# Performance work log

Measured on AMD Instinct MI355X. Metric: run time of the kernel, lower is better.

## Reference

```python
import jax, jax.numpy as jnp
import numpy as np

B, S, H = 2, 1024, 1024
N_IN, N_PROC = 512, 32


def _l2norm(x, eps=1e-12):
    n = jnp.linalg.norm(x, axis=-1, keepdims=True)
    return x / jnp.maximum(n, eps)


def setup_inputs() -> dict:
    key = jax.random.key(0)
    k1, k2, k3, k4 = jax.random.split(key, 4)
    intermediate = jax.random.normal(k1, (B, S, H), dtype=jnp.float32)
    input_activations = jax.random.normal(k2, (B, S, N_IN), dtype=jnp.float32)
    # params (torch defaults: pattern_templates ~ randn; Linear weight ~ U scaled)
    pattern_templates = jax.random.normal(k3, (N_PROC, N_IN), dtype=jnp.float32)
    bound = 1.0 / np.sqrt(H)
    W_transform = jax.random.uniform(k4, (N_PROC * H, H), dtype=jnp.float32,
                                     minval=-bound, maxval=bound)
    return {"intermediate": intermediate, "input_activations": input_activations,
            "pattern_templates": pattern_templates, "W_transform": W_transform}


def reference(intermediate, input_activations, pattern_templates, W_transform):
    # pattern matching -> soft routing weights  [B,S,N_proc]
    act_norm = _l2norm(input_activations)
    tmpl_norm = _l2norm(pattern_templates)
    process_activations = jax.nn.sigmoid(
        jnp.einsum('bsi,ni->bsn', act_norm, tmpl_norm))
    # dispatch: weighted sum over sequence (batched GEMM instead of bcast-mul-sum)
    contexts = jnp.einsum('bsh,bsn->bnh', intermediate, process_activations)
    norm = process_activations.sum(axis=1)[..., None] + 1e-8  # [B,N_proc,1]
    contexts = contexts / norm
    # per-process-neuron HxH transform (torch Linear weight is [out,in])
    Wn = W_transform.reshape(N_PROC, H, H)  # [n, k(out), h(in)]
    transformed = jnp.einsum('bnh,nkh->bnk', contexts, Wn)
    # combine back to tokens  [B,S,H]
    combined = jnp.einsum('bnh,bsn->bsh', transformed, process_activations)
    return combined, process_activations
```

## Files before the change

### kernel.cpp

```cpp
#include <hip/hip_runtime.h>
#include <math.h>

#define B 2
#define S 1024
#define H 1024
#define NIN 512
#define NP 32
#define SC 16
#define SCHUNK (S / SC)

__global__ void k_tmpl_norm(const float* __restrict__ tmpl, float* __restrict__ tn) {
    int n = blockIdx.x;
    int lane = threadIdx.x;
    const float* row = tmpl + (size_t)n * NIN;
    float v[8];
    float ss = 0.f;
#pragma unroll
    for (int k = 0; k < 8; ++k) { v[k] = row[lane + 64 * k]; ss += v[k] * v[k]; }
#pragma unroll
    for (int off = 32; off; off >>= 1) ss += __shfl_down(ss, off);
    ss = __shfl(ss, 0);
    float inv = 1.f / fmaxf(sqrtf(ss), 1e-12f);
#pragma unroll
    for (int k = 0; k < 8; ++k) tn[(size_t)n * NIN + lane + 64 * k] = v[k] * inv;
}

__global__ void k_pattern(const float* __restrict__ act, const float* __restrict__ tn,
                          float* __restrict__ P) {
    __shared__ float act_lds[8][NIN];
    int tid = threadIdx.x;
    int t0 = blockIdx.x * 8;
    {
        const float* src = act + (size_t)t0 * NIN;
        float* dst = &act_lds[0][0];
        for (int k = tid; k < 8 * NIN; k += 256) dst[k] = src[k];
    }
    __syncthreads();
    int tok = tid >> 5;
    int n   = tid & 31;
    float ss = 0.f;
#pragma unroll
    for (int k = 0; k < 16; ++k) { float x = act_lds[tok][n + 32 * k]; ss += x * x; }
#pragma unroll
    for (int m = 16; m; m >>= 1) ss += __shfl_xor(ss, m);
    float inv = 1.f / fmaxf(sqrtf(ss), 1e-12f);
    const float4* t4 = (const float4*)(tn + (size_t)n * NIN);
    const float4* a4 = (const float4*)(&act_lds[tok][0]);
    float d = 0.f;
#pragma unroll 8
    for (int i = 0; i < NIN / 4; ++i) {
        float4 tv = t4[i];
        float4 av = a4[i];
        d += tv.x * av.x + tv.y * av.y + tv.z * av.z + tv.w * av.w;
    }
    d *= inv;
    float p = 1.f / (1.f + expf(-d));
    P[(size_t)(t0 + tok) * NP + n] = p;
}

__global__ void k_norm(const float* __restrict__ P, float* __restrict__ nrm) {
    int bn = blockIdx.x;
    int b = bn >> 5, n = bn & 31;
    int tid = threadIdx.x;
    float s = 0.f;
#pragma unroll
    for (int k = 0; k < 4; ++k) {
        int si = tid + 256 * k;
        s += P[((size_t)b * S + si) * NP + n];
    }
    __shared__ float red[256];
    red[tid] = s;
    __syncthreads();
    for (int off = 128; off >= 1; off >>= 1) {
        if (tid < off) red[tid] += red[tid + off];
        __syncthreads();
    }
    if (tid == 0) nrm[bn] = red[0] + 1e-8f;
}

__global__ void k_ctx_partial(const float* __restrict__ I, const float* __restrict__ P,
                              float* __restrict__ part) {
    int bid = blockIdx.x;
    int ht = bid & 7;
    int sc = (bid >> 3) & (SC - 1);
    int b  = bid >> 7;
    int tid = threadIdx.x;
    __shared__ float Pl[SCHUNK][NP];
    int s0 = sc * SCHUNK;
    {
        const float* src = P + ((size_t)b * S + s0) * NP;
        float* dst = &Pl[0][0];
        for (int k = tid; k < SCHUNK * NP; k += 256) dst[k] = src[k];
    }
    __syncthreads();
    int hl = tid & 127;
    int g  = tid >> 7;
    int h  = ht * 128 + hl;
    float acc[16];
#pragma unroll
    for (int j = 0; j < 16; ++j) acc[j] = 0.f;
    const float* Ip = I + ((size_t)b * S + s0) * H + h;
    for (int s = 0; s < SCHUNK; ++s) {
        float x = Ip[(size_t)s * H];
#pragma unroll
        for (int j = 0; j < 16; ++j) acc[j] += x * Pl[s][g * 16 + j];
    }
    size_t base = (((size_t)b * SC + sc) * NP + g * 16) * H + h;
#pragma unroll
    for (int j = 0; j < 16; ++j) part[base + (size_t)j * H] = acc[j];
}

__global__ void k_ctx_reduce(const float* __restrict__ part, const float* __restrict__ nrm,
                             float* __restrict__ ctx) {
    int idx = blockIdx.x * 256 + threadIdx.x;
    int n = (idx >> 10) & 31;
    int b = idx >> 15;
    float s = 0.f;
#pragma unroll
    for (int sc = 0; sc < SC; ++sc)
        s += part[((size_t)(b * SC + sc) * NP + n) * H + (idx & 1023)];
    ctx[idx] = s / nrm[b * NP + n];
}

__global__ void k_transform(const float* __restrict__ W, const float* __restrict__ ctx,
                            float* __restrict__ T) {
    int bid = blockIdx.x;
    int n  = bid >> 8;
    int kg = bid & 255;
    __shared__ float cl[2 * H];
    int tid = threadIdx.x;
    for (int k = tid; k < 2 * H; k += 256) {
        int b = k >> 10, h = k & 1023;
        cl[k] = ctx[((size_t)b * NP + n) * H + h];
    }
    __syncthreads();
    int w = tid >> 6;
    int lane = tid & 63;
    int kk = kg * 4 + w;
    const float4* Wr = (const float4*)(W + ((size_t)n * H + kk) * H);
    const float4* c0 = (const float4*)(cl);
    const float4* c1 = (const float4*)(cl + H);
    float a0 = 0.f, a1 = 0.f;
#pragma unroll
    for (int it = 0; it < 4; ++it) {
        int idx = it * 64 + lane;
        float4 wv = Wr[idx];
        float4 v0 = c0[idx];
        float4 v1 = c1[idx];
        a0 += wv.x * v0.x + wv.y * v0.y + wv.z * v0.z + wv.w * v0.w;
        a1 += wv.x * v1.x + wv.y * v1.y + wv.z * v1.z + wv.w * v1.w;
    }
#pragma unroll
    for (int off = 32; off; off >>= 1) {
        a0 += __shfl_down(a0, off);
        a1 += __shfl_down(a1, off);
    }
    if (lane == 0) {
        T[(size_t)n * H + kk] = a0;
        T[((size_t)NP + n) * H + kk] = a1;
    }
}

__global__ void k_combine(const float* __restrict__ T, const float* __restrict__ P,
                          float* __restrict__ out) {
    int bid = blockIdx.x;
    int ht = bid & 3;
    int sc = (bid >> 2) & 63;
    int b  = bid >> 8;
    int tid = threadIdx.x;
    __shared__ float Tl[NP][256];
    __shared__ float Pl[16][NP];
    int h0 = ht * 256;
    for (int k = tid; k < NP * 256; k += 256) {
        int n = k >> 8, h = k & 255;
        Tl[n][h] = T[((size_t)b * NP + n) * H + h0 + h];
    }
    int s0 = sc * 16;
    {
        const float* src = P + ((size_t)b * S + s0) * NP;
        float* dst = &Pl[0][0];
        for (int k = tid; k < 16 * NP; k += 256) dst[k] = src[k];
    }
    __syncthreads();
    for (int s = 0; s < 16; ++s) {
        float acc = 0.f;
#pragma unroll
        for (int n = 0; n < NP; ++n) acc += Pl[s][n] * Tl[n][tid];
        out[((size_t)b * S + s0 + s) * H + h0 + tid] = acc;
    }
}

extern "C" void kernel_launch(void* const* d_in, const int* in_sizes, int n_in,
                              void* d_out, int out_size, void* d_ws, size_t ws_size,
                              hipStream_t stream) {
    const float* I    = (const float*)d_in[0];
    const float* act  = (const float*)d_in[1];
    const float* tmpl = (const float*)d_in[2];
    const float* W    = (const float*)d_in[3];
    float* out  = (float*)d_out;
    float* Pout = out + (size_t)B * S * H;

    float* ws   = (float*)d_ws;
    float* tn   = ws;
    float* nrm  = tn + (size_t)NP * NIN;
    float* part = nrm + 64;
    float* ctx  = part + (size_t)B * SC * NP * H;
    float* T    = ctx + (size_t)B * NP * H;

    k_tmpl_norm  <<<NP,                 64, 0, stream>>>(tmpl, tn);
    k_pattern    <<<B * S / 8,         256, 0, stream>>>(act, tn, Pout);
    k_norm       <<<B * NP,            256, 0, stream>>>(Pout, nrm);
    k_ctx_partial<<<B * SC * 8,        256, 0, stream>>>(I, Pout, part);
    k_ctx_reduce <<<B * NP * H / 256,  256, 0, stream>>>(part, nrm, ctx);
    k_transform  <<<NP * 256,          256, 0, stream>>>(W, ctx, T);
    k_combine    <<<B * (S/16) * (H/256), 256, 0, stream>>>(T, Pout, out);
}
```

Baseline: 72.58 us.

## Fuse norm kernels, reduce contexts with atomics, and tile transform over four rows

Folds the template normalization and the routing-weight column sums into the pattern kernel, using an atomic add for the sums. Replaces the partial-context buffer and its reduce kernel with atomic accumulation into ctx, preceded by a memset. The transform now applies the 1/norm scaling itself, keeps ctx in registers, and has each wave compute four output rows, which cuts block count and ctx reloads. This goes from seven launches to four plus a memset, at the cost of atomic contention and non-deterministic summation order.

```diff
diff --git a/kernel.cpp b/kernel.cpp
--- a/kernel.cpp
+++ b/kernel.cpp
@@ -9,33 +9,33 @@
 #define SC 16
 #define SCHUNK (S / SC)
 
-__global__ void k_tmpl_norm(const float* __restrict__ tmpl, float* __restrict__ tn) {
-    int n = blockIdx.x;
-    int lane = threadIdx.x;
-    const float* row = tmpl + (size_t)n * NIN;
-    float v[8];
-    float ss = 0.f;
-#pragma unroll
-    for (int k = 0; k < 8; ++k) { v[k] = row[lane + 64 * k]; ss += v[k] * v[k]; }
-#pragma unroll
-    for (int off = 32; off; off >>= 1) ss += __shfl_down(ss, off);
-    ss = __shfl(ss, 0);
-    float inv = 1.f / fmaxf(sqrtf(ss), 1e-12f);
-#pragma unroll
-    for (int k = 0; k < 8; ++k) tn[(size_t)n * NIN + lane + 64 * k] = v[k] * inv;
-}
-
-__global__ void k_pattern(const float* __restrict__ act, const float* __restrict__ tn,
-                          float* __restrict__ P) {
+__global__ void k_pattern(const float* __restrict__ act, const float* __restrict__ tmpl,
+                          float* __restrict__ P, float* __restrict__ nrm) {
     __shared__ float act_lds[8][NIN];
+    __shared__ float invn[NP];
+    __shared__ float psum[8][NP];
     int tid = threadIdx.x;
     int t0 = blockIdx.x * 8;
+    int b  = t0 >> 10;
+
+    {
+        int n = tid >> 3, sub = tid & 7;
+        const float* tr = tmpl + (size_t)n * NIN;
+        float ss = 0.f;
+#pragma unroll 16
+        for (int k = 0; k < 64; ++k) { float x = tr[sub + 8 * k]; ss += x * x; }
+        ss += __shfl_xor(ss, 1);
+        ss += __shfl_xor(ss, 2);
+        ss += __shfl_xor(ss, 4);
+        if (sub == 0) invn[n] = 1.f / fmaxf(sqrtf(ss), 1e-12f);
+    }
     {
         const float* src = act + (size_t)t0 * NIN;
         float* dst = &act_lds[0][0];
         for (int k = tid; k < 8 * NIN; k += 256) dst[k] = src[k];
     }
     __syncthreads();
+
     int tok = tid >> 5;
     int n   = tid & 31;
     float ss = 0.f;
@@ -43,8 +43,9 @@
     for (int k = 0; k < 16; ++k) { float x = act_lds[tok][n + 32 * k]; ss += x * x; }
 #pragma unroll
     for (int m = 16; m; m >>= 1) ss += __shfl_xor(ss, m);
-    float inv = 1.f / fmaxf(sqrtf(ss), 1e-12f);
-    const float4* t4 = (const float4*)(tn + (size_t)n * NIN);
+    float inva = 1.f / fmaxf(sqrtf(ss), 1e-12f);
+
+    const float4* t4 = (const float4*)(tmpl + (size_t)n * NIN);
     const float4* a4 = (const float4*)(&act_lds[tok][0]);
     float d = 0.f;
 #pragma unroll 8
@@ -53,33 +54,22 @@
         float4 av = a4[i];
         d += tv.x * av.x + tv.y * av.y + tv.z * av.z + tv.w * av.w;
     }
-    d *= inv;
+    d *= inva * invn[n];
     float p = 1.f / (1.f + expf(-d));
     P[(size_t)(t0 + tok) * NP + n] = p;
-}
-
-__global__ void k_norm(const float* __restrict__ P, float* __restrict__ nrm) {
-    int bn = blockIdx.x;
-    int b = bn >> 5, n = bn & 31;
-    int tid = threadIdx.x;
-    float s = 0.f;
-#pragma unroll
-    for (int k = 0; k < 4; ++k) {
-        int si = tid + 256 * k;
-        s += P[((size_t)b * S + si) * NP + n];
-    }
-    __shared__ float red[256];
-    red[tid] = s;
-    __syncthreads();
-    for (int off = 128; off >= 1; off >>= 1) {
-        if (tid < off) red[tid] += red[tid + off];
-        __syncthreads();
-    }
-    if (tid == 0) nrm[bn] = red[0] + 1e-8f;
-}
-
-__global__ void k_ctx_partial(const float* __restrict__ I, const float* __restrict__ P,
-                              float* __restrict__ part) {
+
+    psum[tok][n] = p;
+    __syncthreads();
+    if (tid < NP) {
+        float s = 0.f;
+#pragma unroll
+        for (int t = 0; t < 8; ++t) s += psum[t][tid];
+        unsafeAtomicAdd(&nrm[b * NP + tid], s);
+    }
+}
+
+__global__ void k_ctx(const float* __restrict__ I, const float* __restrict__ P,
+                      float* __restrict__ ctx) {
     int bid = blockIdx.x;
     int ht = bid & 7;
     int sc = (bid >> 3) & (SC - 1);
@@ -105,59 +95,61 @@
 #pragma unroll
         for (int j = 0; j < 16; ++j) acc[j] += x * Pl[s][g * 16 + j];
     }
-    size_t base = (((size_t)b * SC + sc) * NP + g * 16) * H + h;
-#pragma unroll
-    for (int j = 0; j < 16; ++j) part[base + (size_t)j * H] = acc[j];
-}
-
-__global__ void k_ctx_reduce(const float* __restrict__ part, const float* __restrict__ nrm,
-                             float* __restrict__ ctx) {
-    int idx = blockIdx.x * 256 + threadIdx.x;
-    int n = (idx >> 10) & 31;
-    int b = idx >> 15;
-    float s = 0.f;
-#pragma unroll
-    for (int sc = 0; sc < SC; ++sc)
-        s += part[((size_t)(b * SC + sc) * NP + n) * H + (idx & 1023)];
-    ctx[idx] = s / nrm[b * NP + n];
-}
-
-__global__ void k_transform(const float* __restrict__ W, const float* __restrict__ ctx,
-                            float* __restrict__ T) {
+#pragma unroll
+    for (int j = 0; j < 16; ++j)
+        unsafeAtomicAdd(&ctx[((size_t)b * NP + g * 16 + j) * H + h], acc[j]);
+}
+
+__global__ __launch_bounds__(256, 4)
+void k_transform(const float* __restrict__ W, const float* __restrict__ ctx,
+                 const float* __restrict__ nrm, float* __restrict__ T) {
     int bid = blockIdx.x;
-    int n  = bid >> 8;
-    int kg = bid & 255;
-    __shared__ float cl[2 * H];
-    int tid = threadIdx.x;
-    for (int k = tid; k < 2 * H; k += 256) {
-        int b = k >> 10, h = k & 1023;
-        cl[k] = ctx[((size_t)b * NP + n) * H + h];
-    }
-    __syncthreads();
-    int w = tid >> 6;
-    int lane = tid & 63;
-    int kk = kg * 4 + w;
-    const float4* Wr = (const float4*)(W + ((size_t)n * H + kk) * H);
-    const float4* c0 = (const float4*)(cl);
-    const float4* c1 = (const float4*)(cl + H);
-    float a0 = 0.f, a1 = 0.f;
+    int n  = bid >> 6;
+    int rg = bid & 63;
+    int tid = threadIdx.x;
+    int w = tid >> 6, lane = tid & 63;
+
+    float inv0 = 1.f / (nrm[n] + 1e-8f);
+    float inv1 = 1.f / (nrm[NP + n] + 1e-8f);
+
+    const float4* c0g = (const float4*)(ctx + (size_t)n * H);
+    const float4* c1g = (const float4*)(ctx + ((size_t)NP + n) * H);
+    float4 c0[4], c1[4];
 #pragma unroll
     for (int it = 0; it < 4; ++it) {
-        int idx = it * 64 + lane;
-        float4 wv = Wr[idx];
-        float4 v0 = c0[idx];
-        float4 v1 = c1[idx];
-        a0 += wv.x * v0.x + wv.y * v0.y + wv.z * v0.z + wv.w * v0.w;
-        a1 += wv.x * v1.x + wv.y * v1.y + wv.z * v1.z + wv.w * v1.w;
-    }
-#pragma unroll
-    for (int off = 32; off; off >>= 1) {
-        a0 += __shfl_down(a0, off);
-        a1 += __shfl_down(a1, off);
+        float4 v = c0g[it * 64 + lane];
+        c0[it] = make_float4(v.x * inv0, v.y * inv0, v.z * inv0, v.w * inv0);
+        float4 u = c1g[it * 64 + lane];
+        c1[it] = make_float4(u.x * inv1, u.y * inv1, u.z * inv1, u.w * inv1);
+    }
+
+    int row0 = rg * 16 + w * 4;
+    const float4* Wr = (const float4*)(W + ((size_t)n * H + row0) * H);
+    float a0[4] = {0.f, 0.f, 0.f, 0.f};
+    float a1[4] = {0.f, 0.f, 0.f, 0.f};
+#pragma unroll
+    for (int it = 0; it < 4; ++it) {
+#pragma unroll
+        for (int r = 0; r < 4; ++r) {
+            float4 wv = Wr[r * 256 + it * 64 + lane];
+            a0[r] += wv.x * c0[it].x + wv.y * c0[it].y + wv.z * c0[it].z + wv.w * c0[it].w;
+            a1[r] += wv.x * c1[it].x + wv.y * c1[it].y + wv.z * c1[it].z + wv.w * c1[it].w;
+        }
+    }
+#pragma unroll
+    for (int r = 0; r < 4; ++r) {
+#pragma unroll
+        for (int off = 32; off; off >>= 1) {
+            a0[r] += __shfl_xor(a0[r], off);
+            a1[r] += __shfl_xor(a1[r], off);
+        }
     }
     if (lane == 0) {
-        T[(size_t)n * H + kk] = a0;
-        T[((size_t)NP + n) * H + kk] = a1;
+#pragma unroll
+        for (int r = 0; r < 4; ++r) {
+            T[(size_t)n * H + row0 + r] = a0[r];
+            T[((size_t)NP + n) * H + row0 + r] = a1[r];
+        }
     }
 }
 
@@ -200,18 +192,14 @@
     float* out  = (float*)d_out;
     float* Pout = out + (size_t)B * S * H;
 
-    float* ws   = (float*)d_ws;
-    float* tn   = ws;
-    float* nrm  = tn + (size_t)NP * NIN;
-    float* part = nrm + 64;
-    float* ctx  = part + (size_t)B * SC * NP * H;
-    float* T    = ctx + (size_t)B * NP * H;
-
-    k_tmpl_norm  <<<NP,                 64, 0, stream>>>(tmpl, tn);
-    k_pattern    <<<B * S / 8,         256, 0, stream>>>(act, tn, Pout);
-    k_norm       <<<B * NP,            256, 0, stream>>>(Pout, nrm);
-    k_ctx_partial<<<B * SC * 8,        256, 0, stream>>>(I, Pout, part);
-    k_ctx_reduce <<<B * NP * H / 256,  256, 0, stream>>>(part, nrm, ctx);
-    k_transform  <<<NP * 256,          256, 0, stream>>>(W, ctx, T);
-    k_combine    <<<B * (S/16) * (H/256), 256, 0, stream>>>(T, Pout, out);
-}
+    float* ws  = (float*)d_ws;
+    float* ctx = ws;
+    float* nrm = ctx + (size_t)B * NP * H;
+    float* T   = nrm + B * NP;
+
+    hipMemsetAsync(ctx, 0, (size_t)(B * NP * H + B * NP) * sizeof(float), stream);
+    k_pattern  <<<B * S / 8,              256, 0, stream>>>(act, tmpl, Pout, nrm);
+    k_ctx      <<<B * SC * 8,             256, 0, stream>>>(I, Pout, ctx);
+    k_transform<<<NP * 64,                256, 0, stream>>>(W, ctx, nrm, T);
+    k_combine  <<<B * (S/16) * (H/256),   256, 0, stream>>>(T, Pout, out);
+}
```

After: 78.91 us. +8.7%, slower.
